# Optimization experiments

Measured on AMD Instinct MI355X. Metric: run time of the kernel, lower is better.

The kernel has to match this reference:

```python
import jax, jax.numpy as jnp
import numpy as np

# Hardcoded capability requirements per task (3 capabilities x 13 tasks), as in the source.
CAP_MATRIX = 0.01 * np.array([
    [0.0, 33.0, 50.0, 43.0, 56.0, 67.0, 62.0, 47.0, 50.0, 51.0, 64.0, 64.0, 68.0],
    [0.0, 33.0, 49.0, 39.0, 58.0, 67.0, 60.0, 54.0, 52.0, 52.0, 67.0, 69.0, 71.0],
    [0.0, 33.0, 42.0, 39.0, 44.0, 52.0, 49.0, 42.0, 45.0, 46.0, 52.0, 53.0, 56.0],
], dtype=np.float32)  # [3, 13]

T_TASKS = 64      # tasks per observation sequence
B_SEQS = 262144   # number of observation sequences
N_TASK_IDS = 13
CAP_DIM = 3


def setup_inputs() -> dict:
    key = jax.random.key(0)
    k1, k2, k3, k4, k5 = jax.random.split(key, 5)
    # Performance encoding must avoid the invalid (1,1) combo:
    # state 0 -> (0,0) no info; state 1 -> (0,1) success; state 2 -> (1,0) failure.
    state = jax.random.randint(k1, (T_TASKS, B_SEQS), 0, 3)
    inptasksperf = jnp.stack(
        [(state == 2).astype(jnp.int32), (state == 1).astype(jnp.int32)], axis=-1
    )  # [T, B, 2]
    tasksobsids = jax.random.randint(k2, (T_TASKS, B_SEQS, 1), 0, N_TASK_IDS).astype(jnp.int32)
    taskspredids = jax.random.randint(k3, (B_SEQS, 1), 0, N_TASK_IDS).astype(jnp.int32)
    inptasksobs = jnp.zeros((T_TASKS, B_SEQS, 1), jnp.float32)  # only shapes are used
    betas = 20.0 * jax.random.uniform(k4, (CAP_DIM,), jnp.float32)
    zetas = jax.random.uniform(k5, (CAP_DIM,), jnp.float32)
    return {
        "inptasksobs": inptasksobs,
        "inptasksperf": inptasksperf,
        "tasksobsids": tasksobsids,
        "taskspredids": taskspredids,
        "num_obs_tasks": T_TASKS,
        "betas": betas,
        "zetas": zetas,
    }


def reference(inptasksobs, inptasksperf, tasksobsids, taskspredids, num_obs_tasks, betas, zetas):
    cap_table = jnp.asarray(CAP_MATRIX.T)                # [13, 3] per-task capability rows
    obs_cap = cap_table[tasksobsids[..., 0]]             # [T, B, 3]
    p0 = inptasksperf[..., 0] != 0                       # [T, B]
    p1 = inptasksperf[..., 1] != 0
    success = jnp.logical_and(~p0, p1)                   # (0,1) -> success
    failure = jnp.logical_and(p0, ~p1)                   # (1,0) -> failure; (0,0) -> skip

    def step(cap, x):
        oc, s, f = x                                     # oc [B,3], s/f [B]
        cap = jnp.where(s[:, None], jnp.maximum(cap, oc), cap)
        cap = jnp.where(f[:, None], jnp.minimum(cap, oc), cap)
        return cap, None

    cap0 = jnp.zeros((obs_cap.shape[1], CAP_DIM), jnp.float32)
    cap, _ = jax.lax.scan(step, cap0, (obs_cap, success, failure))  # [B, 3]

    req = cap_table[taskspredids[:, 0]]                  # [B, 3]
    p = betas * (req - cap)                              # [B, 3]
    trust = jnp.prod((1.0 + jnp.exp(p)) ** (-zetas), axis=-1, keepdims=True)  # [B, 1]
    return trust
```

## Files before the change

### kernel.cpp

```cpp
#include <hip/hip_runtime.h>

#define T_TASKS 64
#define B_SEQS 262144
#define BLOCK 256
#define CHUNKS 8
#define TPC 8
#define PAIRS 32

#define POS_BIG  3.402823466e+38f
#define NEG_BIG -3.402823466e+38f

typedef int   v4i __attribute__((ext_vector_type(4)));
typedef int   v2i __attribute__((ext_vector_type(2)));

__constant__ float c_capT[13][4] = {
    {0.00f, 0.00f, 0.00f, 0.f}, {0.33f, 0.33f, 0.33f, 0.f},
    {0.50f, 0.49f, 0.42f, 0.f}, {0.43f, 0.39f, 0.39f, 0.f},
    {0.56f, 0.58f, 0.44f, 0.f}, {0.67f, 0.67f, 0.52f, 0.f},
    {0.62f, 0.60f, 0.49f, 0.f}, {0.47f, 0.54f, 0.42f, 0.f},
    {0.50f, 0.52f, 0.45f, 0.f}, {0.51f, 0.52f, 0.46f, 0.f},
    {0.64f, 0.67f, 0.52f, 0.f}, {0.64f, 0.69f, 0.53f, 0.f},
    {0.68f, 0.71f, 0.56f, 0.f},
};

#define STEP(l, h, A, B)                          \
    l = __builtin_amdgcn_fmed3f(l, A, B);         \
    h = __builtin_amdgcn_fmed3f(h, A, B);

#define GLOAD4(dst, ptr) \
    asm volatile("global_load_dwordx4 %0, %1, off" : "=v"(dst) : "v"(ptr))
#define GLOAD2(dst, ptr) \
    asm volatile("global_load_dwordx2 %0, %1, off" : "=v"(dst) : "v"(ptr))

__global__ __launch_bounds__(BLOCK, 4) void trust_kernel(
    const v4i* __restrict__ perf2,
    const v2i* __restrict__ obs2,
    const int* __restrict__ predids,
    const float* __restrict__ betas,
    const float* __restrict__ zetas,
    float* __restrict__ out)
{
    __shared__ float4 s_cap[13];
    __shared__ float  s_lh[CHUNKS][2 * PAIRS][7];

    if (threadIdx.x < 13)
        s_cap[threadIdx.x] = *(const float4*)&c_capT[threadIdx.x][0];
    __syncthreads();

    const int tid = threadIdx.x;
    const int ps  = tid & (PAIRS - 1);
    const int c   = tid >> 5;
    const size_t rowStride = B_SEQS / 2;
    const size_t pair = (size_t)blockIdx.x * PAIRS + ps;
    const size_t base = (size_t)(c * TPC) * rowStride + pair;

    v4i pf0, pf1, pf2, pf3, pf4, pf5, pf6, pf7;
    v2i id0, id1, id2, id3, id4, id5, id6, id7;
    {
        const v4i* a = perf2 + base;
        GLOAD4(pf0, a);  a += rowStride;
        GLOAD4(pf1, a);  a += rowStride;
        GLOAD4(pf2, a);  a += rowStride;
        GLOAD4(pf3, a);  a += rowStride;
        GLOAD4(pf4, a);  a += rowStride;
        GLOAD4(pf5, a);  a += rowStride;
        GLOAD4(pf6, a);  a += rowStride;
        GLOAD4(pf7, a);
        const v2i* b = obs2 + base;
        GLOAD2(id0, b);  b += rowStride;
        GLOAD2(id1, b);  b += rowStride;
        GLOAD2(id2, b);  b += rowStride;
        GLOAD2(id3, b);  b += rowStride;
        GLOAD2(id4, b);  b += rowStride;
        GLOAD2(id5, b);  b += rowStride;
        GLOAD2(id6, b);  b += rowStride;
        GLOAD2(id7, b);
    }
    asm volatile("s_waitcnt vmcnt(0)" ::: "memory");
    __builtin_amdgcn_sched_barrier(0);

    float la0=NEG_BIG, la1=NEG_BIG, la2=NEG_BIG;
    float ha0=POS_BIG, ha1=POS_BIG, ha2=POS_BIG;
    float lb0=NEG_BIG, lb1=NEG_BIG, lb2=NEG_BIG;
    float hb0=POS_BIG, hb1=POS_BIG, hb2=POS_BIG;

#define CONSUME(pf, idv)                                                     \
    {                                                                        \
        const float4 oa = s_cap[(idv).x];                                    \
        const float4 ob = s_cap[(idv).y];                                    \
        const bool sa = ((pf).x == 0) && ((pf).y != 0);                      \
        const bool fa = ((pf).x != 0) && ((pf).y == 0);                      \
        const bool sb = ((pf).z == 0) && ((pf).w != 0);                      \
        const bool fb = ((pf).z != 0) && ((pf).w == 0);                      \
        const float Aa0 = sa ? oa.x : NEG_BIG, Ba0 = fa ? oa.x : POS_BIG;    \
        const float Aa1 = sa ? oa.y : NEG_BIG, Ba1 = fa ? oa.y : POS_BIG;    \
        const float Aa2 = sa ? oa.z : NEG_BIG, Ba2 = fa ? oa.z : POS_BIG;    \
        const float Ab0 = sb ? ob.x : NEG_BIG, Bb0 = fb ? ob.x : POS_BIG;    \
        const float Ab1 = sb ? ob.y : NEG_BIG, Bb1 = fb ? ob.y : POS_BIG;    \
        const float Ab2 = sb ? ob.z : NEG_BIG, Bb2 = fb ? ob.z : POS_BIG;    \
        STEP(la0, ha0, Aa0, Ba0)                                             \
        STEP(la1, ha1, Aa1, Ba1)                                             \
        STEP(la2, ha2, Aa2, Ba2)                                             \
        STEP(lb0, hb0, Ab0, Bb0)                                             \
        STEP(lb1, hb1, Ab1, Bb1)                                             \
        STEP(lb2, hb2, Ab2, Bb2)                                             \
    }

    CONSUME(pf0, id0)
    CONSUME(pf1, id1)
    CONSUME(pf2, id2)
    CONSUME(pf3, id3)
    CONSUME(pf4, id4)
    CONSUME(pf5, id5)
    CONSUME(pf6, id6)
    CONSUME(pf7, id7)
#undef CONSUME

    float* da = &s_lh[c][2 * ps][0];
    da[0]=la0; da[1]=la1; da[2]=la2; da[3]=ha0; da[4]=ha1; da[5]=ha2;
    float* db = &s_lh[c][2 * ps + 1][0];
    db[0]=lb0; db[1]=lb1; db[2]=lb2; db[3]=hb0; db[4]=hb1; db[5]=hb2;
    __syncthreads();

    if (tid < 2 * PAIRS) {
        float x0 = 0.0f, x1 = 0.0f, x2 = 0.0f;
        #pragma unroll
        for (int cc = 0; cc < CHUNKS; ++cc) {
            const float* q = &s_lh[cc][tid][0];
            x0 = fminf(fmaxf(x0, q[0]), q[3]);
            x1 = fminf(fmaxf(x1, q[1]), q[4]);
            x2 = fminf(fmaxf(x2, q[2]), q[5]);
        }
        const size_t seq = (size_t)blockIdx.x * (2 * PAIRS) + tid;
        const int pid = predids[seq];
        const float4 r = s_cap[pid];

        const float q0 = betas[0] * (r.x - x0);
        const float q1 = betas[1] * (r.y - x1);
        const float q2 = betas[2] * (r.z - x2);

        const float t0 = powf(1.0f + expf(q0), -zetas[0]);
        const float t1 = powf(1.0f + expf(q1), -zetas[1]);
        const float t2 = powf(1.0f + expf(q2), -zetas[2]);

        out[seq] = t0 * t1 * t2;
    }
}

extern "C" void kernel_launch(void* const* d_in, const int* in_sizes, int n_in,
                              void* d_out, int out_size, void* d_ws, size_t ws_size,
                              hipStream_t stream) {
    const v4i*   perf2   = (const v4i*)d_in[1];
    const v2i*   obs2    = (const v2i*)d_in[2];
    const int*   predids = (const int*)d_in[3];
    const float* betas   = (const float*)d_in[5];
    const float* zetas   = (const float*)d_in[6];
    float* out = (float*)d_out;

    const int blocks = B_SEQS / (2 * PAIRS);
    trust_kernel<<<blocks, BLOCK, 0, stream>>>(perf2, obs2, predids, betas, zetas, out);
}
```

Measured before the change: 269.0 us.

## Pipeline global loads with a rolling 4-slot buffer and wider per-wave pair tiles

Each wave now covers 64 contiguous pairs across 16 timesteps instead of 32 pairs across 8. Loads go through a four-deep register ring with partial vmcnt waits, so min/max consumption overlaps outstanding loads. This is meant to increase memory-level parallelism per thread, improve coalescing to full-wave contiguous rows, and halve the number of blocks. The trade-off is fewer loads in flight at once per thread (4 instead of 8) and a longer serial chain per thread.

```diff
diff --git a/kernel.cpp b/kernel.cpp
--- a/kernel.cpp
+++ b/kernel.cpp
@@ -3,15 +3,15 @@
 #define T_TASKS 64
 #define B_SEQS 262144
 #define BLOCK 256
-#define CHUNKS 8
-#define TPC 8
-#define PAIRS 32
+#define CHUNKS 4
+#define TPC 16
+#define PAIRS 64
 
 #define POS_BIG  3.402823466e+38f
 #define NEG_BIG -3.402823466e+38f
 
-typedef int   v4i __attribute__((ext_vector_type(4)));
-typedef int   v2i __attribute__((ext_vector_type(2)));
+typedef int v4i __attribute__((ext_vector_type(4)));
+typedef int v2i __attribute__((ext_vector_type(2)));
 
 __constant__ float c_capT[13][4] = {
     {0.00f, 0.00f, 0.00f, 0.f}, {0.33f, 0.33f, 0.33f, 0.f},
@@ -31,6 +31,9 @@
     asm volatile("global_load_dwordx4 %0, %1, off" : "=v"(dst) : "v"(ptr))
 #define GLOAD2(dst, ptr) \
     asm volatile("global_load_dwordx2 %0, %1, off" : "=v"(dst) : "v"(ptr))
+#define WAITC(N)                                                  \
+    asm volatile("s_waitcnt vmcnt(" #N ")" ::: "memory");         \
+    __builtin_amdgcn_sched_barrier(0);
 
 __global__ __launch_bounds__(BLOCK, 4) void trust_kernel(
     const v4i* __restrict__ perf2,
@@ -48,36 +51,20 @@
     __syncthreads();
 
     const int tid = threadIdx.x;
-    const int ps  = tid & (PAIRS - 1);
-    const int c   = tid >> 5;
-    const size_t rowStride = B_SEQS / 2;
-    const size_t pair = (size_t)blockIdx.x * PAIRS + ps;
-    const size_t base = (size_t)(c * TPC) * rowStride + pair;
+    const int wv  = tid >> 6;
+    const int ln  = tid & 63;
+    const size_t RS = B_SEQS / 2;
+    const size_t pairBase = (size_t)blockIdx.x * PAIRS;
 
-    v4i pf0, pf1, pf2, pf3, pf4, pf5, pf6, pf7;
-    v2i id0, id1, id2, id3, id4, id5, id6, id7;
-    {
-        const v4i* a = perf2 + base;
-        GLOAD4(pf0, a);  a += rowStride;
-        GLOAD4(pf1, a);  a += rowStride;
-        GLOAD4(pf2, a);  a += rowStride;
-        GLOAD4(pf3, a);  a += rowStride;
-        GLOAD4(pf4, a);  a += rowStride;
-        GLOAD4(pf5, a);  a += rowStride;
-        GLOAD4(pf6, a);  a += rowStride;
-        GLOAD4(pf7, a);
-        const v2i* b = obs2 + base;
-        GLOAD2(id0, b);  b += rowStride;
-        GLOAD2(id1, b);  b += rowStride;
-        GLOAD2(id2, b);  b += rowStride;
-        GLOAD2(id3, b);  b += rowStride;
-        GLOAD2(id4, b);  b += rowStride;
-        GLOAD2(id5, b);  b += rowStride;
-        GLOAD2(id6, b);  b += rowStride;
-        GLOAD2(id7, b);
-    }
-    asm volatile("s_waitcnt vmcnt(0)" ::: "memory");
-    __builtin_amdgcn_sched_barrier(0);
+    const v4i* ap = perf2 + (size_t)(wv * TPC) * RS + pairBase + ln;
+    const v2i* bp = obs2  + (size_t)(wv * TPC) * RS + pairBase + ln;
+
+    v4i pfs0, pfs1, pfs2, pfs3;
+    v2i ids0, ids1, ids2, ids3;
+
+#define ISSUE(S)                                   \
+    GLOAD4(pfs##S, ap);  ap += RS;                 \
+    GLOAD2(ids##S, bp);  bp += RS;
 
     float la0=NEG_BIG, la1=NEG_BIG, la2=NEG_BIG;
     float ha0=POS_BIG, ha1=POS_BIG, ha2=POS_BIG;
@@ -106,19 +93,29 @@
         STEP(lb2, hb2, Ab2, Bb2)                                             \
     }
 
-    CONSUME(pf0, id0)
-    CONSUME(pf1, id1)
-    CONSUME(pf2, id2)
-    CONSUME(pf3, id3)
-    CONSUME(pf4, id4)
-    CONSUME(pf5, id5)
-    CONSUME(pf6, id6)
-    CONSUME(pf7, id7)
+    ISSUE(0) ISSUE(1) ISSUE(2) ISSUE(3)
+    WAITC(6) CONSUME(pfs0, ids0) ISSUE(0)
+    WAITC(6) CONSUME(pfs1, ids1) ISSUE(1)
+    WAITC(6) CONSUME(pfs2, ids2) ISSUE(2)
+    WAITC(6) CONSUME(pfs3, ids3) ISSUE(3)
+    WAITC(6) CONSUME(pfs0, ids0) ISSUE(0)
+    WAITC(6) CONSUME(pfs1, ids1) ISSUE(1)
+    WAITC(6) CONSUME(pfs2, ids2) ISSUE(2)
+    WAITC(6) CONSUME(pfs3, ids3) ISSUE(3)
+    WAITC(6) CONSUME(pfs0, ids0) ISSUE(0)
+    WAITC(6) CONSUME(pfs1, ids1) ISSUE(1)
+    WAITC(6) CONSUME(pfs2, ids2) ISSUE(2)
+    WAITC(6) CONSUME(pfs3, ids3) ISSUE(3)
+    WAITC(6) CONSUME(pfs0, ids0)
+    WAITC(4) CONSUME(pfs1, ids1)
+    WAITC(2) CONSUME(pfs2, ids2)
+    WAITC(0) CONSUME(pfs3, ids3)
 #undef CONSUME
+#undef ISSUE
 
-    float* da = &s_lh[c][2 * ps][0];
+    float* da = &s_lh[wv][2 * ln][0];
     da[0]=la0; da[1]=la1; da[2]=la2; da[3]=ha0; da[4]=ha1; da[5]=ha2;
-    float* db = &s_lh[c][2 * ps + 1][0];
+    float* db = &s_lh[wv][2 * ln + 1][0];
     db[0]=lb0; db[1]=lb1; db[2]=lb2; db[3]=hb0; db[4]=hb1; db[5]=hb2;
     __syncthreads();
 
```

Measured after the change: 267.5 us. No clear change (-0.6%).
